# Kernel tuning notes

Hardware: AMD Instinct MI355X
Metric: run time of the kernel (lower is better)

## Reference

```python
import jax, jax.numpy as jnp
import numpy as np

MAX_DELTAS = 4
PACK = 8  # 4-bit values packed into int32
HIDDEN = 4096
Q_SLICE = 4096   # num_heads(32) * head_size(128)
KV_SLICE = 1024  # num_kv_heads(8) * head_size(128)
TOKENS = 4096


def setup_inputs() -> dict:
    key = jax.random.key(0)
    ks = jax.random.split(key, 16)
    imax = 2**31 - 1
    inp = {
        "x": jax.random.normal(ks[0], (TOKENS, HIDDEN), dtype=jnp.float32),
        "base_weight": jax.random.normal(ks[1], (Q_SLICE + 2 * KV_SLICE, HIDDEN), dtype=jnp.float32) * 0.02,
        "qweight_q": jax.random.randint(ks[2], (MAX_DELTAS, 1, HIDDEN // PACK, Q_SLICE), 0, imax, dtype=jnp.int32),
        "qweight_k": jax.random.randint(ks[3], (MAX_DELTAS, 1, HIDDEN // PACK, KV_SLICE), 0, imax, dtype=jnp.int32),
        "qweight_v": jax.random.randint(ks[4], (MAX_DELTAS, 1, HIDDEN // PACK, KV_SLICE), 0, imax, dtype=jnp.int32),
        "qzeros_q": jax.random.randint(ks[5], (MAX_DELTAS, 1, 1, Q_SLICE // PACK), 0, imax, dtype=jnp.int32),
        "qzeros_k": jax.random.randint(ks[6], (MAX_DELTAS, 1, 1, KV_SLICE // PACK), 0, imax, dtype=jnp.int32),
        "qzeros_v": jax.random.randint(ks[7], (MAX_DELTAS, 1, 1, KV_SLICE // PACK), 0, imax, dtype=jnp.int32),
        "scales_q": jax.random.uniform(ks[8], (MAX_DELTAS, 1, 1, Q_SLICE), dtype=jnp.float32) * 0.01,
        "scales_k": jax.random.uniform(ks[9], (MAX_DELTAS, 1, 1, KV_SLICE), dtype=jnp.float32) * 0.01,
        "scales_v": jax.random.uniform(ks[10], (MAX_DELTAS, 1, 1, KV_SLICE), dtype=jnp.float32) * 0.01,
        "indices": jax.random.randint(ks[11], (TOKENS,), 0, MAX_DELTAS, dtype=jnp.int32),
    }
    return inp


def _unpack_rows(qw):
    # (D, 1, K//PACK, N) int32 -> (D, K, N) 4-bit values, packed along K
    D, _, Kp, N = qw.shape
    shifts = (jnp.arange(PACK, dtype=jnp.int32) * 4)
    q = (qw[:, 0, :, None, :] >> shifts[None, None, :, None]) & 0xF  # (D,Kp,PACK,N)
    return q.reshape(D, Kp * PACK, N)


def _unpack_cols(qz):
    # (D, 1, 1, N//PACK) int32 -> (D, N), packed along N
    D = qz.shape[0]
    shifts = (jnp.arange(PACK, dtype=jnp.int32) * 4)
    z = (qz[:, 0, 0, :, None] >> shifts[None, None, :]) & 0xF  # (D, N//PACK, PACK)
    return z.reshape(D, -1)


def _dequant(qw, qz, sc):
    # GPTQ-style dequant, single group (g_idx is all zeros): W = (q - (z+1)) * scale
    q = _unpack_rows(qw).astype(jnp.float32)            # (D, K, N)
    z = (_unpack_cols(qz) + 1).astype(jnp.float32)      # (D, N)
    return (q - z[:, None, :]) * sc[:, 0, 0, :][:, None, :]


def _delta_slice(x, indices, qw, qz, sc):
    # per-token indexed delta matmul: out[t] = x[t] @ W[indices[t]] (0 if index==-1)
    W = _dequant(qw, qz, sc)  # (D, K, N)
    out = jnp.zeros((x.shape[0], W.shape[2]), dtype=x.dtype)
    for d in range(MAX_DELTAS):
        mask = (indices == d).astype(x.dtype)[:, None]
        out = out + (x * mask) @ W[d]
    return out


def reference(x, base_weight, qweight_q, qweight_k, qweight_v,
              qzeros_q, qzeros_k, qzeros_v,
              scales_q, scales_k, scales_v, indices):
    # base merged QKV projection
    base_out = x @ base_weight.T  # (T, q + 2*kv)
    # per-slice delta adds (offsets handled by concatenation order: q, k, v)
    dq = _delta_slice(x, indices, qweight_q, qzeros_q, scales_q)
    dk = _delta_slice(x, indices, qweight_k, qzeros_k, scales_k)
    dv = _delta_slice(x, indices, qweight_v, qzeros_v, scales_v)
    return base_out + jnp.concatenate([dq, dk, dv], axis=1)
```

## Files before the change

kernel.cpp:

```cpp
#include <hip/hip_runtime.h>
#include <stdint.h>

#define TOKENS 4096
#define HIDDEN 4096
#define NQ     4096
#define NKV    1024
#define NTOT   6144
#define KPACK  512
#define MAXTILES 36

typedef __attribute__((ext_vector_type(8))) __bf16 bf16x8;
typedef __attribute__((ext_vector_type(8))) short short8v;
typedef __attribute__((ext_vector_type(4))) float floatx4;

__device__ __forceinline__ short f2bf(float f) {
  union { float f; unsigned u; } v; v.f = f;
  unsigned r = v.u + 0x7fffu + ((v.u >> 16) & 1u);
  return (short)(r >> 16);
}

__device__ __forceinline__ void load_lds16(const void* g, void* l) {
  __builtin_amdgcn_global_load_lds((__attribute__((address_space(1))) void*)(g),
                                   (__attribute__((address_space(3))) void*)(l),
                                   16, 0, 0);
}

__global__ __launch_bounds__(256) void prep_tokens(const int* __restrict__ idx,
                                                   int* __restrict__ token_list,
                                                   int* __restrict__ grp) {
  __shared__ int cnt[4], cur[4];
  const int tid = threadIdx.x;
  if (tid < 4) cnt[tid] = 0;
  __syncthreads();
  for (int t = tid; t < TOKENS; t += 256) {
    int d = idx[t];
    if ((unsigned)d < 4u) atomicAdd(&cnt[d], 1);
  }
  __syncthreads();
  if (tid == 0) {
    int s = 0, nt = 0;
    for (int d = 0; d < 4; d++) {
      cur[d] = s; grp[d] = s; grp[4 + d] = cnt[d]; s += cnt[d];
      int tiles = (cnt[d] + 127) >> 7;
      for (int rt = 0; rt < tiles; rt++) grp[9 + nt++] = d | (rt << 2);
    }
    grp[8] = nt;
  }
  __syncthreads();
  for (int t = tid; t < TOKENS; t += 256) {
    int d = idx[t];
    if ((unsigned)d < 4u) {
      int p = atomicAdd(&cur[d], 1);
      token_list[p] = t;
    }
  }
}

__global__ __launch_bounds__(256) void cvt_x(const float* __restrict__ x,
                                             short* __restrict__ xb) {
  size_t g = (size_t)blockIdx.x * 256 + threadIdx.x;
  size_t i = g * 8;
  float4 a = ((const float4*)(x + i))[0];
  float4 b = ((const float4*)(x + i))[1];
  short8v o;
  o[0] = f2bf(a.x); o[1] = f2bf(a.y); o[2] = f2bf(a.z); o[3] = f2bf(a.w);
  o[4] = f2bf(b.x); o[5] = f2bf(b.y); o[6] = f2bf(b.z); o[7] = f2bf(b.w);
  *(short8v*)(xb + i) = o;
}

__global__ __launch_bounds__(256) void combine_w(
    const float* __restrict__ bw,
    const int* __restrict__ qwq, const int* __restrict__ qwk, const int* __restrict__ qwv,
    const int* __restrict__ qzq, const int* __restrict__ qzk, const int* __restrict__ qzv,
    const float* __restrict__ scq, const float* __restrict__ sck, const float* __restrict__ scv,
    short* __restrict__ wc) {
  __shared__ int ldsq[4][8][72];
  __shared__ float zs[4][64], ss[4][64];
  const int tid = threadIdx.x;
  const int n0  = blockIdx.y * 64;
  const int kp0 = blockIdx.x * 8;

  const int* qw; const int* qz; const float* sc; int Ns, nb;
  if (n0 < NQ)            { qw = qwq; qz = qzq; sc = scq; Ns = NQ;  nb = n0; }
  else if (n0 < NQ + NKV) { qw = qwk; qz = qzk; sc = sck; Ns = NKV; nb = n0 - NQ; }
  else                    { qw = qwv; qz = qzv; sc = scv; Ns = NKV; nb = n0 - NQ - NKV; }

  {
    int d = tid >> 6, n = tid & 63;
    int nn = nb + n;
    int z = (int)(((unsigned)qz[d * (Ns >> 3) + (nn >> 3)] >> ((nn & 7) * 4)) & 0xFu);
    zs[d][n] = (float)(z + 1);
    ss[d][n] = sc[d * Ns + nn];
  }

#pragma unroll
  for (int d = 0; d < 4; d++) {
#pragma unroll
    for (int p = 0; p < 2; p++) {
      int i  = tid + p * 256;
      int kp = i >> 6, n = i & 63;
      ldsq[d][kp][n] = qw[((size_t)d * KPACK + kp0 + kp) * Ns + nb + n];
    }
  }
  __syncthreads();

  const int kp = tid & 7;
#pragma unroll
  for (int p = 0; p < 2; p++) {
    int n = (tid >> 3) + p * 32;
    const float4* bp = (const float4*)(bw + (size_t)(n0 + n) * HIDDEN + (kp0 + kp) * 8);
    float4 b0 = bp[0], b1 = bp[1];
    float bv[8] = {b0.x, b0.y, b0.z, b0.w, b1.x, b1.y, b1.z, b1.w};
#pragma unroll
    for (int d = 0; d < 4; d++) {
      unsigned q32 = (unsigned)ldsq[d][kp][n];
      float z = zs[d][n], s = ss[d][n];
      short8v o;
#pragma unroll
      for (int j = 0; j < 8; j++)
        o[j] = f2bf(((float)((q32 >> (4 * j)) & 0xFu) - z) * s + bv[j]);
      *(short8v*)(wc + ((size_t)d * NTOT + n0 + n) * HIDDEN + (kp0 + kp) * 8) = o;
    }
  }
}

__global__ __launch_bounds__(256, 2) void gemm_grouped(
    const short* __restrict__ xb, const short* __restrict__ wc,
    const int* __restrict__ token_list, const int* __restrict__ grp,
    float* __restrict__ out) {
  const int nt = grp[8];
  if ((int)blockIdx.y >= nt) return;
  const int te = grp[9 + blockIdx.y];
  const int d  = te & 3;
  const int rt = te >> 2;
  const int cnt   = grp[4 + d];
  const int start = grp[d];
  const int n0 = blockIdx.x * 256;

  __shared__ __align__(16) short As[128 * 32];
  __shared__ __align__(16) short Bs[256 * 32];
  __shared__ int toks[128];

  const int tid = threadIdx.x;
  if (tid < 128) {
    int r = rt * 128 + tid;
    if (r >= cnt) r = cnt - 1;
    toks[tid] = token_list[start + r];
  }
  __syncthreads();

  const int wave = tid >> 6;
  const int lane = tid & 63;

  const int sw = ((lane & 3) ^ ((lane >> 3) & 3)) * 8;

  const int arow0 = wave * 32 + (lane >> 2);
  const short* gA0 = xb + (size_t)toks[arow0] * HIDDEN + sw;
  const short* gA1 = xb + (size_t)toks[arow0 + 16] * HIDDEN + sw;
  short* lA0 = As + (size_t)wave * 1024;
  short* lA1 = lA0 + 512;

  const short* wrow = wc + ((size_t)d * NTOT + n0) * HIDDEN;
  const int brow0 = wave * 64 + (lane >> 2);
  const short* gB0 = wrow + (size_t)brow0 * HIDDEN + sw;
  const short* gB1 = gB0 + (size_t)16 * HIDDEN;
  const short* gB2 = gB0 + (size_t)32 * HIDDEN;
  const short* gB3 = gB0 + (size_t)48 * HIDDEN;
  short* lB0 = Bs + (size_t)wave * 2048;
  short* lB1 = lB0 + 512;
  short* lB2 = lB0 + 1024;
  short* lB3 = lB0 + 1536;

  const int mrow = lane & 15;
  const int sx = (((lane >> 4) ^ ((mrow >> 1) & 3))) * 8;
  const int wm = (wave >> 1) * 64;
  const int wn = (wave & 1) * 128;

  floatx4 acc[4][8];
#pragma unroll
  for (int i = 0; i < 4; i++)
#pragma unroll
    for (int j = 0; j < 8; j++) acc[i][j] = (floatx4){0.f, 0.f, 0.f, 0.f};

  for (int k0 = 0; k0 < HIDDEN; k0 += 32) {
    load_lds16(gA0 + k0, lA0);
    load_lds16(gA1 + k0, lA1);
    load_lds16(gB0 + k0, lB0);
    load_lds16(gB1 + k0, lB1);
    load_lds16(gB2 + k0, lB2);
    load_lds16(gB3 + k0, lB3);
    __syncthreads();

    bf16x8 a[4], b[8];
#pragma unroll
    for (int i = 0; i < 4; i++)
      a[i] = *(const bf16x8*)(As + (wm + i * 16 + mrow) * 32 + sx);
#pragma unroll
    for (int j = 0; j < 8; j++)
      b[j] = *(const bf16x8*)(Bs + (wn + j * 16 + mrow) * 32 + sx);
#pragma unroll
    for (int i = 0; i < 4; i++)
#pragma unroll
      for (int j = 0; j < 8; j++)
        acc[i][j] = __builtin_amdgcn_mfma_f32_16x16x32_bf16(a[i], b[j], acc[i][j], 0, 0, 0);
    __syncthreads();
  }

  const int rbase = (lane >> 4) * 4;
  const int coll  = lane & 15;
#pragma unroll
  for (int i = 0; i < 4; i++) {
#pragma unroll
    for (int r = 0; r < 4; r++) {
      int m = wm + i * 16 + rbase + r;
      if (rt * 128 + m < cnt) {
        float* orow = out + (size_t)toks[m] * NTOT + n0 + wn + coll;
#pragma unroll
        for (int j = 0; j < 8; j++) orow[j * 16] = acc[i][j][r];
      }
    }
  }
}

extern "C" void kernel_launch(void* const* d_in, const int* in_sizes, int n_in,
                              void* d_out, int out_size, void* d_ws, size_t ws_size,
                              hipStream_t stream) {
  const float* x   = (const float*)d_in[0];
  const float* bw  = (const float*)d_in[1];
  const int*   qwq = (const int*)d_in[2];
  const int*   qwk = (const int*)d_in[3];
  const int*   qwv = (const int*)d_in[4];
  const int*   qzq = (const int*)d_in[5];
  const int*   qzk = (const int*)d_in[6];
  const int*   qzv = (const int*)d_in[7];
  const float* scq = (const float*)d_in[8];
  const float* sck = (const float*)d_in[9];
  const float* scv = (const float*)d_in[10];
  const int*   idx = (const int*)d_in[11];
  float* out = (float*)d_out;

  char* ws = (char*)d_ws;
  short* xb = (short*)ws;
  short* wc = (short*)(ws + (size_t)33554432);
  int* token_list = (int*)(ws + (size_t)33554432 + 201326592);
  int* grp = token_list + TOKENS;

  prep_tokens<<<1, 256, 0, stream>>>(idx, token_list, grp);
  cvt_x<<<(TOKENS * HIDDEN) / (256 * 8), 256, 0, stream>>>(x, xb);
  dim3 gc(HIDDEN / 64, NTOT / 64);
  combine_w<<<gc, 256, 0, stream>>>(bw, qwq, qwk, qwv, qzq, qzk, qzv, scq, sck, scv, wc);
  dim3 gg(NTOT / 256, MAXTILES);
  gemm_grouped<<<gg, 256, 0, stream>>>(xb, wc, token_list, grp, out);
}
```

Before: 587.3 us.

## Double-buffer LDS tiles in grouped GEMM to overlap loads with MFMA

Splits the shared-memory A and B tiles into two buffers and restructures the K loop to stage the next K-slice via global_load_lds while computing on the current one. This aims to hide global memory latency behind MFMA work instead of serialising load then compute each iteration. It doubles LDS usage per block, which may pressure occupancy at two blocks per CU.

```diff
diff --git a/kernel.cpp b/kernel.cpp
--- a/kernel.cpp
+++ b/kernel.cpp
@@ -123,6 +123,38 @@
     }
   }
 }
+
+__device__ __forceinline__ void stage_tile(const short* gA0, const short* gA1,
+                                           const short* gB0, const short* gB1,
+                                           const short* gB2, const short* gB3,
+                                           int k0, short* aDst, short* bDst) {
+  load_lds16(gA0 + k0, aDst);
+  load_lds16(gA1 + k0, aDst + 512);
+  load_lds16(gB0 + k0, bDst);
+  load_lds16(gB1 + k0, bDst + 512);
+  load_lds16(gB2 + k0, bDst + 1024);
+  load_lds16(gB3 + k0, bDst + 1536);
+}
+
+__device__ __forceinline__ void compute_tile(const short* Ab, const short* Bb,
+                                             int wm, int wn, int mrow, int sx,
+                                             floatx4 acc[4][8]) {
+  bf16x8 a[4], b[8];
+#pragma unroll
+  for (int i = 0; i < 4; i++)
+    a[i] = *(const bf16x8*)(Ab + (wm + i * 16 + mrow) * 32 + sx);
+#pragma unroll
+  for (int j = 0; j < 8; j++)
+    b[j] = *(const bf16x8*)(Bb + (wn + j * 16 + mrow) * 32 + sx);
+#pragma unroll
+  for (int i = 0; i < 4; i++)
+#pragma unroll
+    for (int j = 0; j < 8; j++)
+      acc[i][j] = __builtin_amdgcn_mfma_f32_16x16x32_bf16(a[i], b[j], acc[i][j], 0, 0, 0);
+}
+
+#define A_BUF 4096
+#define B_BUF 8192
 
 __global__ __launch_bounds__(256, 2) void gemm_grouped(
     const short* __restrict__ xb, const short* __restrict__ wc,
@@ -137,8 +169,8 @@
   const int start = grp[d];
   const int n0 = blockIdx.x * 256;
 
-  __shared__ __align__(16) short As[128 * 32];
-  __shared__ __align__(16) short Bs[256 * 32];
+  __shared__ __align__(16) short As[2 * A_BUF];
+  __shared__ __align__(16) short Bs[2 * B_BUF];
   __shared__ int toks[128];
 
   const int tid = threadIdx.x;
@@ -157,8 +189,7 @@
   const int arow0 = wave * 32 + (lane >> 2);
   const short* gA0 = xb + (size_t)toks[arow0] * HIDDEN + sw;
   const short* gA1 = xb + (size_t)toks[arow0 + 16] * HIDDEN + sw;
-  short* lA0 = As + (size_t)wave * 1024;
-  short* lA1 = lA0 + 512;
+  short* lA = As + (size_t)wave * 1024;
 
   const short* wrow = wc + ((size_t)d * NTOT + n0) * HIDDEN;
   const int brow0 = wave * 64 + (lane >> 2);
@@ -166,10 +197,7 @@
   const short* gB1 = gB0 + (size_t)16 * HIDDEN;
   const short* gB2 = gB0 + (size_t)32 * HIDDEN;
   const short* gB3 = gB0 + (size_t)48 * HIDDEN;
-  short* lB0 = Bs + (size_t)wave * 2048;
-  short* lB1 = lB0 + 512;
-  short* lB2 = lB0 + 1024;
-  short* lB3 = lB0 + 1536;
+  short* lB = Bs + (size_t)wave * 2048;
 
   const int mrow = lane & 15;
   const int sx = (((lane >> 4) ^ ((mrow >> 1) & 3))) * 8;
@@ -182,27 +210,17 @@
 #pragma unroll
     for (int j = 0; j < 8; j++) acc[i][j] = (floatx4){0.f, 0.f, 0.f, 0.f};
 
-  for (int k0 = 0; k0 < HIDDEN; k0 += 32) {
-    load_lds16(gA0 + k0, lA0);
-    load_lds16(gA1 + k0, lA1);
-    load_lds16(gB0 + k0, lB0);
-    load_lds16(gB1 + k0, lB1);
-    load_lds16(gB2 + k0, lB2);
-    load_lds16(gB3 + k0, lB3);
+  stage_tile(gA0, gA1, gB0, gB1, gB2, gB3, 0, lA, lB);
+  __syncthreads();
+
+  for (int k0 = 0; k0 < HIDDEN; k0 += 64) {
+    stage_tile(gA0, gA1, gB0, gB1, gB2, gB3, k0 + 32, lA + A_BUF, lB + B_BUF);
+    compute_tile(As, Bs, wm, wn, mrow, sx, acc);
     __syncthreads();
 
-    bf16x8 a[4], b[8];
-#pragma unroll
-    for (int i = 0; i < 4; i++)
-      a[i] = *(const bf16x8*)(As + (wm + i * 16 + mrow) * 32 + sx);
-#pragma unroll
-    for (int j = 0; j < 8; j++)
-      b[j] = *(const bf16x8*)(Bs + (wn + j * 16 + mrow) * 32 + sx);
-#pragma unroll
-    for (int i = 0; i < 4; i++)
-#pragma unroll
-      for (int j = 0; j < 8; j++)
-        acc[i][j] = __builtin_amdgcn_mfma_f32_16x16x32_bf16(a[i], b[j], acc[i][j], 0, 0, 0);
+    if (k0 + 64 < HIDDEN)
+      stage_tile(gA0, gA1, gB0, gB1, gB2, gB3, k0 + 64, lA, lB);
+    compute_tile(As + A_BUF, Bs + B_BUF, wm, wn, mrow, sx, acc);
     __syncthreads();
   }
 
```

Result: slower. 602.8 us (+2.6%).

## Enlarge grouped GEMM tile to 256x256 with 4-stage LDS pipeline

Applied to the files above, without the earlier changes.

The grouped GEMM goes from 128-row tiles with 256 threads and a single LDS buffer to 256-row tiles with 512 threads and a four-buffer LDS ring. Async global-to-LDS loads run two stages ahead, gated by explicit vmcnt waits and one barrier per k-step, and setprio is raised around the MFMA bursts. The aim is to hide global load latency, drop the second barrier per iteration, and raise compute per loaded byte. The cost is 128KB of LDS per block, which likely allows only one block per CU, and more padded rows on each group's last tile.

```diff
diff --git a/kernel.cpp b/kernel.cpp
--- a/kernel.cpp
+++ b/kernel.cpp
@@ -7,7 +7,7 @@
 #define NKV    1024
 #define NTOT   6144
 #define KPACK  512
-#define MAXTILES 36
+#define MAXTILES 20
 
 typedef __attribute__((ext_vector_type(8))) __bf16 bf16x8;
 typedef __attribute__((ext_vector_type(8))) short short8v;
@@ -24,6 +24,8 @@
                                    (__attribute__((address_space(3))) void*)(l),
                                    16, 0, 0);
 }
+
+#define VMCNT(n) asm volatile("s_waitcnt vmcnt(" #n ")" ::: "memory")
 
 __global__ __launch_bounds__(256) void prep_tokens(const int* __restrict__ idx,
                                                    int* __restrict__ token_list,
@@ -41,7 +43,7 @@
     int s = 0, nt = 0;
     for (int d = 0; d < 4; d++) {
       cur[d] = s; grp[d] = s; grp[4 + d] = cnt[d]; s += cnt[d];
-      int tiles = (cnt[d] + 127) >> 7;
+      int tiles = (cnt[d] + 255) >> 8;
       for (int rt = 0; rt < tiles; rt++) grp[9 + nt++] = d | (rt << 2);
     }
     grp[8] = nt;
@@ -124,7 +126,62 @@
   }
 }
 
-__global__ __launch_bounds__(256, 2) void gemm_grouped(
+__device__ __forceinline__ void stage_t(int t, short* aBuf, short* bBuf,
+                                        const short* gA0, const short* gA1,
+                                        const short* gB0, const short* gB1,
+                                        int wave) {
+  const int ko = t * 32;
+  short* la = aBuf + wave * 512;
+  short* lb = bBuf + wave * 512;
+  load_lds16(gA0 + ko, la);
+  load_lds16(gA1 + ko, la + 4096);
+  load_lds16(gB0 + ko, lb);
+  load_lds16(gB1 + ko, lb + 4096);
+}
+
+__device__ __forceinline__ void compute_tile(const short* Ab, const short* Bb,
+                                             int wm, int wn, int mrow, int sx,
+                                             floatx4 acc[8][4]) {
+  bf16x8 bfr[4], afr[4];
+#pragma unroll
+  for (int j = 0; j < 4; j++)
+    bfr[j] = *(const bf16x8*)(Bb + (wn * 64 + j * 16 + mrow) * 32 + sx);
+#pragma unroll
+  for (int i = 0; i < 4; i++)
+    afr[i] = *(const bf16x8*)(Ab + (wm * 128 + i * 16 + mrow) * 32 + sx);
+  __builtin_amdgcn_s_setprio(1);
+#pragma unroll
+  for (int i = 0; i < 4; i++)
+#pragma unroll
+    for (int j = 0; j < 4; j++)
+      acc[i][j] = __builtin_amdgcn_mfma_f32_16x16x32_bf16(afr[i], bfr[j], acc[i][j], 0, 0, 0);
+  __builtin_amdgcn_s_setprio(0);
+#pragma unroll
+  for (int i = 0; i < 4; i++)
+    afr[i] = *(const bf16x8*)(Ab + (wm * 128 + (i + 4) * 16 + mrow) * 32 + sx);
+  __builtin_amdgcn_s_setprio(1);
+#pragma unroll
+  for (int i = 0; i < 4; i++)
+#pragma unroll
+    for (int j = 0; j < 4; j++)
+      acc[i + 4][j] = __builtin_amdgcn_mfma_f32_16x16x32_bf16(afr[i], bfr[j], acc[i + 4][j], 0, 0, 0);
+  __builtin_amdgcn_s_setprio(0);
+}
+
+#define GSTEP(CUR, NXT, TNXT, VM)                                     \
+  stage_t(TNXT, &As[NXT][0], &Bs[NXT][0], gA0, gA1, gB0, gB1, wave);  \
+  VMCNT(VM);                                                          \
+  __builtin_amdgcn_s_barrier();                                       \
+  __builtin_amdgcn_sched_barrier(0);                                  \
+  compute_tile(&As[CUR][0], &Bs[CUR][0], wm, wn, mrow, sx, acc);
+
+#define GSTEP_NOST(CUR, VM)                                           \
+  VMCNT(VM);                                                          \
+  __builtin_amdgcn_s_barrier();                                       \
+  __builtin_amdgcn_sched_barrier(0);                                  \
+  compute_tile(&As[CUR][0], &Bs[CUR][0], wm, wn, mrow, sx, acc);
+
+__global__ __launch_bounds__(512, 2) void gemm_grouped(
     const short* __restrict__ xb, const short* __restrict__ wc,
     const int* __restrict__ token_list, const int* __restrict__ grp,
     float* __restrict__ out) {
@@ -137,13 +194,13 @@
   const int start = grp[d];
   const int n0 = blockIdx.x * 256;
 
-  __shared__ __align__(16) short As[128 * 32];
-  __shared__ __align__(16) short Bs[256 * 32];
-  __shared__ int toks[128];
+  __shared__ __align__(16) short As[4][8192];
+  __shared__ __align__(16) short Bs[4][8192];
+  __shared__ int toks[256];
 
   const int tid = threadIdx.x;
-  if (tid < 128) {
-    int r = rt * 128 + tid;
+  if (tid < 256) {
+    int r = rt * 256 + tid;
     if (r >= cnt) r = cnt - 1;
     toks[tid] = token_list[start + r];
   }
@@ -154,69 +211,50 @@
 
   const int sw = ((lane & 3) ^ ((lane >> 3) & 3)) * 8;
 
-  const int arow0 = wave * 32 + (lane >> 2);
-  const short* gA0 = xb + (size_t)toks[arow0] * HIDDEN + sw;
-  const short* gA1 = xb + (size_t)toks[arow0 + 16] * HIDDEN + sw;
-  short* lA0 = As + (size_t)wave * 1024;
-  short* lA1 = lA0 + 512;
-
+  const int arow = wave * 16 + (lane >> 2);
+  const short* gA0 = xb + (size_t)toks[arow] * HIDDEN + sw;
+  const short* gA1 = xb + (size_t)toks[arow + 128] * HIDDEN + sw;
   const short* wrow = wc + ((size_t)d * NTOT + n0) * HIDDEN;
-  const int brow0 = wave * 64 + (lane >> 2);
-  const short* gB0 = wrow + (size_t)brow0 * HIDDEN + sw;
-  const short* gB1 = gB0 + (size_t)16 * HIDDEN;
-  const short* gB2 = gB0 + (size_t)32 * HIDDEN;
-  const short* gB3 = gB0 + (size_t)48 * HIDDEN;
-  short* lB0 = Bs + (size_t)wave * 2048;
-  short* lB1 = lB0 + 512;
-  short* lB2 = lB0 + 1024;
-  short* lB3 = lB0 + 1536;
+  const short* gB0 = wrow + (size_t)arow * HIDDEN + sw;
+  const short* gB1 = gB0 + (size_t)128 * HIDDEN;
 
   const int mrow = lane & 15;
   const int sx = (((lane >> 4) ^ ((mrow >> 1) & 3))) * 8;
-  const int wm = (wave >> 1) * 64;
-  const int wn = (wave & 1) * 128;
-
-  floatx4 acc[4][8];
-#pragma unroll
-  for (int i = 0; i < 4; i++)
-#pragma unroll
-    for (int j = 0; j < 8; j++) acc[i][j] = (floatx4){0.f, 0.f, 0.f, 0.f};
-
-  for (int k0 = 0; k0 < HIDDEN; k0 += 32) {
-    load_lds16(gA0 + k0, lA0);
-    load_lds16(gA1 + k0, lA1);
-    load_lds16(gB0 + k0, lB0);
-    load_lds16(gB1 + k0, lB1);
-    load_lds16(gB2 + k0, lB2);
-    load_lds16(gB3 + k0, lB3);
-    __syncthreads();
-
-    bf16x8 a[4], b[8];
-#pragma unroll
-    for (int i = 0; i < 4; i++)
-      a[i] = *(const bf16x8*)(As + (wm + i * 16 + mrow) * 32 + sx);
-#pragma unroll
-    for (int j = 0; j < 8; j++)
-      b[j] = *(const bf16x8*)(Bs + (wn + j * 16 + mrow) * 32 + sx);
-#pragma unroll
-    for (int i = 0; i < 4; i++)
-#pragma unroll
-      for (int j = 0; j < 8; j++)
-        acc[i][j] = __builtin_amdgcn_mfma_f32_16x16x32_bf16(a[i], b[j], acc[i][j], 0, 0, 0);
-    __syncthreads();
-  }
+  const int wm = wave >> 2;
+  const int wn = wave & 3;
+
+  floatx4 acc[8][4];
+#pragma unroll
+  for (int i = 0; i < 8; i++)
+#pragma unroll
+    for (int j = 0; j < 4; j++) acc[i][j] = (floatx4){0.f, 0.f, 0.f, 0.f};
+
+  stage_t(0, &As[0][0], &Bs[0][0], gA0, gA1, gB0, gB1, wave);
+  stage_t(1, &As[1][0], &Bs[1][0], gA0, gA1, gB0, gB1, wave);
+
+  for (int it = 0; it < 31; ++it) {
+    const int t = it * 4;
+    GSTEP(0, 2, t + 2, 8);
+    GSTEP(1, 3, t + 3, 8);
+    GSTEP(2, 0, t + 4, 8);
+    GSTEP(3, 1, t + 5, 8);
+  }
+  GSTEP(0, 2, 126, 8);
+  GSTEP(1, 3, 127, 8);
+  GSTEP_NOST(2, 4);
+  GSTEP_NOST(3, 0);
 
   const int rbase = (lane >> 4) * 4;
   const int coll  = lane & 15;
 #pragma unroll
-  for (int i = 0; i < 4; i++) {
+  for (int i = 0; i < 8; i++) {
 #pragma unroll
     for (int r = 0; r < 4; r++) {
-      int m = wm + i * 16 + rbase + r;
-      if (rt * 128 + m < cnt) {
-        float* orow = out + (size_t)toks[m] * NTOT + n0 + wn + coll;
-#pragma unroll
-        for (int j = 0; j < 8; j++) orow[j * 16] = acc[i][j][r];
+      int m = wm * 128 + i * 16 + rbase + r;
+      if (rt * 256 + m < cnt) {
+        float* orow = out + (size_t)toks[m] * NTOT + n0 + wn * 64 + coll;
+#pragma unroll
+        for (int j = 0; j < 4; j++) orow[j * 16] = acc[i][j][r];
       }
     }
   }
@@ -250,5 +288,5 @@
   dim3 gc(HIDDEN / 64, NTOT / 64);
   combine_w<<<gc, 256, 0, stream>>>(bw, qwq, qwk, qwv, qzq, qzk, qzv, scq, sck, scv, wc);
   dim3 gg(NTOT / 256, MAXTILES);
-  gemm_grouped<<<gg, 256, 0, stream>>>(xb, wc, token_list, grp, out);
-}
+  gemm_grouped<<<gg, 512, 0, stream>>>(xb, wc, token_list, grp, out);
+}
```

Measured after the change: 570.3 us. 1.03x faster.
